# Optimization experiments

Hardware: AMD Instinct MI355X
Metric: run time of the kernel (lower is better)

## Reference

```python
import jax, jax.numpy as jnp
import numpy as np
from jax import lax

B, L, D, H = 32, 32, 512, 512
NEG = jnp.float32(-1e9)


def setup_inputs() -> dict:
    key = jax.random.key(0)
    k1, k2, k3, k4, k5 = jax.random.split(key, 5)
    return {
        "inp": jax.random.normal(k1, (B, L, D), jnp.float32),
        "length": jax.random.randint(k2, (B,), 2, L + 1),
        "W_word": jax.random.normal(k3, (D, 2 * H), jnp.float32) * np.float32(np.sqrt(2.0 / D)),
        "b_word": jnp.zeros((2 * H,), jnp.float32),
        "W_comp": jax.random.normal(k4, (2 * H, 5 * H), jnp.float32) * np.float32(np.sqrt(2.0 / (2 * H))),
        "b_comp": jnp.zeros((5 * H,), jnp.float32),
        "comp_query": jax.random.normal(k5, (H,), jnp.float32) * np.float32(0.01),
    }


def _forward(inp, length, W_word, b_word, W_comp, b_comp, comp_query):
    # length_mask[b, t] = 1 if t < length[b]
    length_mask = (jnp.arange(L)[None, :] < length[:, None]).astype(jnp.float32)  # (B, L)
    # leaf states from word_linear: (B, L, 2H) -> h, c
    hc = inp @ W_word + b_word
    h0, c0 = jnp.split(hc, 2, axis=-1)  # each (B, L, H)

    def cell(hl, cl, hr, cr):
        # BinaryTreeLSTMLayer: cat -> 5H gates
        g = jnp.concatenate([hl, hr], axis=-1) @ W_comp + b_comp  # (B, L-1, 5H)
        ig, fl, fr, u, o = jnp.split(g, 5, axis=-1)
        c = cl * jax.nn.sigmoid(fl + 1.0) + cr * jax.nn.sigmoid(fr + 1.0) + jnp.tanh(u) * jax.nn.sigmoid(ig)
        h = jax.nn.sigmoid(o) * jnp.tanh(c)
        return h, c

    def step(carry, i):
        # Fixed-shape (B, L, H) carry; valid length shrinks by 1 each step,
        # tail is zero-padded garbage never selected thanks to masks.
        h, c = carry
        hl, hr = h[:, :-1, :], h[:, 1:, :]
        cl, cr = c[:, :-1, :], c[:, 1:, :]
        nh, nc = cell(hl, cl, hr, cr)  # (B, L-1, H) candidate parents
        # greedy (eval-mode) top-1 composition selection
        logits = jnp.einsum('blh,h->bl', nh, comp_query)
        cand = (jnp.arange(L - 1)[None, :] < (length[:, None] - 1 - i)).astype(jnp.float32)
        sel = jax.nn.one_hot(jnp.argmax(jnp.where(cand > 0, logits, NEG), axis=1), L - 1, dtype=jnp.float32)
        cum = jnp.cumsum(sel, axis=1)
        left = 1.0 - cum
        right = jnp.concatenate([jnp.zeros((B, 1), jnp.float32), cum[:, :-1]], axis=1)
        ch = sel[..., None] * nh + left[..., None] * hl + right[..., None] * hr
        cc = sel[..., None] * nc + left[..., None] * cl + right[..., None] * cr
        sel_h = jnp.sum(sel[..., None] * ch, axis=1)  # (B, H) selected composed node
        is_last = (i == L - 2)  # final merge skips selection (single candidate)
        uh = jnp.where(is_last, nh, ch)
        uc = jnp.where(is_last, nc, cc)
        done = length_mask[:, i + 1][:, None, None]  # 1 if this sample still merging
        nhst = done * uh + (1.0 - done) * h[:, :-1, :]
        ncst = done * uc + (1.0 - done) * c[:, :-1, :]
        pad = jnp.zeros((B, 1, H), jnp.float32)
        h2 = jnp.concatenate([nhst, pad], axis=1)
        c2 = jnp.concatenate([ncst, pad], axis=1)
        node = jnp.where(is_last, h2[:, 0, :], sel_h)
        return (h2, c2), node

    (hf, cf), nodes_rest = lax.scan(step, (h0, c0), jnp.arange(L - 1))
    nodes = jnp.concatenate([h0, jnp.swapaxes(nodes_rest, 0, 1)], axis=1)  # (B, 2L-1, H)
    return hf[:, 0, :], cf[:, 0, :], nodes


def reference(inp, length, W_word, b_word, W_comp, b_comp, comp_query):
    return _forward(inp, length, W_word, b_word, W_comp, b_comp, comp_query)
```

## Files before the change

### kernel.cpp

```cpp
#include <hip/hip_runtime.h>
#include <math.h>

constexpr int NB = 32, NL = 32, ND = 512, NHID = 512, NSTEPS = 31;
constexpr int NC5 = 2560;
constexpr int BH = NB * NHID;
constexpr int HSLOT_Z = 32;
constexpr int NBLK = 160;
constexpr int NGEMM = 80;

constexpr float INV2048 = 1.f / 2048.f;

typedef _Float16 half8  __attribute__((ext_vector_type(8)));
typedef _Float16 half4  __attribute__((ext_vector_type(4)));
typedef float    f32x16 __attribute__((ext_vector_type(16)));
typedef unsigned long long u64;

constexpr size_t OFF_GRAW = 0;
constexpr size_t OFF_PNH  = OFF_GRAW + (size_t)32 * 32 * 2560;
constexpr size_t OFF_PNC  = OFF_PNH + (size_t)31 * 32 * 512;
constexpr size_t OFF_CST  = OFF_PNC + (size_t)31 * 32 * 512;
constexpr size_t OFF_HHI  = OFF_CST + (size_t)33 * 32 * 512;
constexpr size_t OFF_HLO  = OFF_HHI + (size_t)64 * 32 * 512 / 2;
constexpr size_t OFF_WTH  = OFF_HLO + (size_t)64 * 32 * 512 / 2;
constexpr size_t OFF_WTL  = OFF_WTH + (size_t)NC5 * 1024 / 2;
constexpr size_t OFF_INT  = OFF_WTL + (size_t)NC5 * 1024 / 2;
constexpr size_t OFF_LIST = OFF_INT + 8192;

__device__ __forceinline__ float sigf(float x) { return 1.f / (1.f + expf(-x)); }

__device__ __forceinline__ int ld_sc(const int* p) {
    return __hip_atomic_load(p, __ATOMIC_RELAXED, __HIP_MEMORY_SCOPE_AGENT);
}
__device__ __forceinline__ u64 ld_sc64(const void* p) {
    return __hip_atomic_load((const u64*)p, __ATOMIC_RELAXED, __HIP_MEMORY_SCOPE_AGENT);
}
__device__ __forceinline__ void st_sc64(void* p, u64 v) {
    __hip_atomic_store((u64*)p, v, __ATOMIC_RELAXED, __HIP_MEMORY_SCOPE_AGENT);
}
__device__ __forceinline__ u64 packf2(float a, float b) {
    return (u64)__float_as_uint(a) | ((u64)__float_as_uint(b) << 32);
}
__device__ __forceinline__ float2 uf2(u64 v) {
    float2 r;
    r.x = __uint_as_float((unsigned)v);
    r.y = __uint_as_float((unsigned)(v >> 32));
    return r;
}

__device__ __forceinline__ unsigned pack_e(int b, int slot, int l, int r) {
    return (unsigned)b | ((unsigned)slot << 5) | ((unsigned)l << 10) | ((unsigned)r << 16);
}

__global__ __launch_bounds__(256) void init_kernel(
    int* __restrict__ ireg, u64* __restrict__ elist,
    _Float16* __restrict__ hHi, _Float16* __restrict__ hLo, float* __restrict__ cSt)
{
    const int blk = blockIdx.x, tid = threadIdx.x;
    if (blk < 32) {
        if (tid < 31) {
            unsigned e = (unsigned)blk | ((unsigned)tid << 5) |
                         ((unsigned)tid << 10) | ((unsigned)(tid + 1) << 16);
            elist[tid * 32 + blk] = (u64)e;
        }
    } else if (blk == 32) {
        const size_t zb = (size_t)HSLOT_Z * NB * NHID;
        for (int i = tid; i < NB * NHID; i += 256) {
            hHi[zb + i] = (_Float16)0.f;
            hLo[zb + i] = (_Float16)0.f;
            cSt[zb + i] = 0.f;
        }
    } else {
        for (int i = tid; i < 8192; i += 256) ireg[i] = 0;
    }
}

__global__ __launch_bounds__(256) void wsplit_kernel(
    const float* __restrict__ W, _Float16* __restrict__ Wth, _Float16* __restrict__ Wtl)
{
    __shared__ float t[32][33];
    const int n0 = blockIdx.x * 32, k0 = blockIdx.y * 32;
    const int tid = threadIdx.x;
    const int c = tid & 31, r8 = tid >> 5;
#pragma unroll
    for (int p = 0; p < 4; ++p) {
        int r = p * 8 + r8;
        t[r][c] = W[(size_t)(k0 + r) * NC5 + n0 + c];
    }
    __syncthreads();
    const int nl = tid >> 3, k4 = (tid & 7) * 4;
    half4 vh, vl;
#pragma unroll
    for (int i = 0; i < 4; ++i) {
        float v = t[k4 + i][nl];
        _Float16 hh = (_Float16)v;
        vh[i] = hh;
        vl[i] = (_Float16)((v - (float)hh) * 2048.f);
    }
    size_t o = (size_t)(n0 + nl) * 1024 + k0 + k4;
    *(half4*)&Wth[o] = vh;
    *(half4*)&Wtl[o] = vl;
}

__global__ __launch_bounds__(256) void word_gemm64(
    const float* __restrict__ A, const float* __restrict__ W,
    const float* __restrict__ bias,
    _Float16* __restrict__ hi0, _Float16* __restrict__ lo0,
    float* __restrict__ cst, float* __restrict__ out)
{
    const int m0 = blockIdx.x * 64;
    const int n0 = blockIdx.y * 64;
    const int tid = threadIdx.x;
    const int tx = tid & 15, ty = tid >> 4;
    __shared__ float As[16][64];
    __shared__ float Bs[16][64];
    float acc[4][4];
#pragma unroll
    for (int i = 0; i < 4; ++i)
#pragma unroll
        for (int j = 0; j < 4; ++j) acc[i][j] = 0.f;

    for (int kt = 0; kt < ND; kt += 16) {
        {
            int row = tid >> 2, kq = tid & 3;
            float4 v = *(const float4*)(A + (size_t)(m0 + row) * ND + kt + kq * 4);
            As[kq * 4 + 0][row] = v.x;
            As[kq * 4 + 1][row] = v.y;
            As[kq * 4 + 2][row] = v.z;
            As[kq * 4 + 3][row] = v.w;
            int kr = tid >> 4, nq = tid & 15;
            float4 vb = *(const float4*)(W + (size_t)(kt + kr) * 1024 + n0 + nq * 4);
            *(float4*)&Bs[kr][nq * 4] = vb;
        }
        __syncthreads();
#pragma unroll
        for (int kk = 0; kk < 16; ++kk) {
            float a0 = As[kk][ty * 4 + 0], a1 = As[kk][ty * 4 + 1];
            float a2 = As[kk][ty * 4 + 2], a3 = As[kk][ty * 4 + 3];
            float4 bv = *(float4*)&Bs[kk][tx * 4];
            acc[0][0] = fmaf(a0, bv.x, acc[0][0]); acc[0][1] = fmaf(a0, bv.y, acc[0][1]);
            acc[0][2] = fmaf(a0, bv.z, acc[0][2]); acc[0][3] = fmaf(a0, bv.w, acc[0][3]);
            acc[1][0] = fmaf(a1, bv.x, acc[1][0]); acc[1][1] = fmaf(a1, bv.y, acc[1][1]);
            acc[1][2] = fmaf(a1, bv.z, acc[1][2]); acc[1][3] = fmaf(a1, bv.w, acc[1][3]);
            acc[2][0] = fmaf(a2, bv.x, acc[2][0]); acc[2][1] = fmaf(a2, bv.y, acc[2][1]);
            acc[2][2] = fmaf(a2, bv.z, acc[2][2]); acc[2][3] = fmaf(a2, bv.w, acc[2][3]);
            acc[3][0] = fmaf(a3, bv.x, acc[3][0]); acc[3][1] = fmaf(a3, bv.y, acc[3][1]);
            acc[3][2] = fmaf(a3, bv.z, acc[3][2]); acc[3][3] = fmaf(a3, bv.w, acc[3][3]);
        }
        __syncthreads();
    }
    float* nodes = out + 2 * BH;
#pragma unroll
    for (int i = 0; i < 4; ++i) {
        int r = m0 + ty * 4 + i;
        int b = r >> 5, l = r & 31;
#pragma unroll
        for (int jn = 0; jn < 4; ++jn) {
            int n = n0 + tx * 4 + jn;
            float v = acc[i][jn] + bias[n];
            if (n < NHID) {
                size_t si = ((size_t)l * NB + b) * NHID + n;
                _Float16 hh = (_Float16)v;
                hi0[si] = hh;
                lo0[si] = (_Float16)((v - (float)hh) * 2048.f);
                nodes[((size_t)b * 63 + l) * NHID + n] = v;
            } else {
                cst[((size_t)l * NB + b) * NHID + (n - NHID)] = v;
            }
        }
    }
}

__global__ __launch_bounds__(256, 1) void tree_loop(
    _Float16* __restrict__ hHi, _Float16* __restrict__ hLo,
    const _Float16* __restrict__ Wth, const _Float16* __restrict__ Wtl,
    float* __restrict__ graw, const float* __restrict__ bias,
    const float* __restrict__ q, const int* __restrict__ len,
    float* __restrict__ pnh, float* __restrict__ pnc, float* __restrict__ cSt,
    u64* __restrict__ elist, int* __restrict__ ireg, float* __restrict__ out)
{
    const int nt = blockIdx.x;
    const int tid = threadIdx.x;
    const int col = nt % NGEMM;
    const int kw = tid >> 6;
    const int lane = tid & 63;
    const int l5 = lane >> 5, ln = lane & 31;

    int* gd = ireg;

    __shared__ float red[4][32][32];
    __shared__ unsigned s_entry[64];
    __shared__ int s_pidx[32], s_hidx[32], s_cidx[32];
    __shared__ float s_plog[32];
    __shared__ int s_k;
    __shared__ int s_prevk;

    const _Float16* bHiP = Wth + (size_t)(col * 32 + ln) * 1024 + (kw << 8) + l5 * 8;
    const _Float16* bLoP = Wtl + (size_t)(col * 32 + ln) * 1024 + (kw << 8) + l5 * 8;
    half8 Bh[16], Bl[16];
#pragma unroll
    for (int ks = 0; ks < 16; ++ks) {
        Bh[ks] = *(const half8*)(bHiP + ks * 16);
        Bl[ks] = *(const half8*)(bLoP + ks * 16);
    }

    auto gemm_tile = [&](const unsigned* se) {
        {
            const unsigned e = se[ln];
            const int db = e & 31;
            const int lsl = (e >> 10) & 63, rsl = (e >> 16) & 63;
            const int hs = (kw < 2) ? lsl : rsl;
            const int koff = ((kw & 1) << 8) + l5 * 8;
            const _Float16* aHiP = hHi + ((size_t)hs * NB + db) * NHID + koff;
            const _Float16* aLoP = hLo + ((size_t)hs * NB + db) * NHID + koff;
            f32x16 acc1 = (f32x16)0.f, acc2 = (f32x16)0.f;
#pragma unroll
            for (int ks = 0; ks < 16; ++ks) {
                half8 Ah = *(const half8*)(aHiP + ks * 16);
                half8 Al = *(const half8*)(aLoP + ks * 16);
                acc1 = __builtin_amdgcn_mfma_f32_32x32x16_f16(Ah, Bh[ks], acc1, 0, 0, 0);
                acc2 = __builtin_amdgcn_mfma_f32_32x32x16_f16(Ah, Bl[ks], acc2, 0, 0, 0);
                acc2 = __builtin_amdgcn_mfma_f32_32x32x16_f16(Al, Bh[ks], acc2, 0, 0, 0);
            }
#pragma unroll
            for (int a = 0; a < 16; ++a) {
                int row = (a & 3) + 8 * (a >> 2) + 4 * l5;
                red[kw][row][ln] = acc1[a] + acc2[a] * INV2048;
            }
        }
        __syncthreads();
        {
            const int row = tid >> 3, c0 = (tid & 7) * 4;
            const unsigned er = se[row];
            const int rb = er & 31, rslot = (er >> 5) & 31;
            float4 s;
            s.x = (red[0][row][c0+0] + red[1][row][c0+0]) + (red[2][row][c0+0] + red[3][row][c0+0]);
            s.y = (red[0][row][c0+1] + red[1][row][c0+1]) + (red[2][row][c0+1] + red[3][row][c0+1]);
            s.z = (red[0][row][c0+2] + red[1][row][c0+2]) + (red[2][row][c0+2] + red[3][row][c0+2]);
            s.w = (red[0][row][c0+3] + red[1][row][c0+3]) + (red[2][row][c0+3] + red[3][row][c0+3]);
            float* gp = &graw[((size_t)rslot * NB + rb) * NC5 + col * 32 + c0];
            st_sc64(gp,     packf2(s.x, s.y));
            st_sc64(gp + 2, packf2(s.z, s.w));
        }
        __syncthreads();
    };

    __syncthreads();
    {
        const int par = nt / NGEMM;
        for (int mt = par; mt < 31; mt += 2) {
            if (tid < 32) s_entry[tid] = (unsigned)ld_sc64(&elist[mt * 32 + tid]);
            __syncthreads();
            gemm_tile(s_entry);
        }
        if (tid == 0) {
            asm volatile("s_waitcnt vmcnt(0)" ::: "memory");
            __hip_atomic_fetch_add(&gd[(nt & 3) * 32], 1, __ATOMIC_RELAXED,
                                   __HIP_MEMORY_SCOPE_AGENT);
        }
    }
    if (nt >= 112) return;

    if (nt < NGEMM) {
        for (int step = 1; step < NSTEPS; ++step) {
            if (tid < 64) {
                u64 e;
                while ((int)((e = ld_sc64(&elist[tid])) >> 32) < step)
                    __builtin_amdgcn_s_sleep(1);
                s_entry[tid] = (unsigned)e;
            }
            __syncthreads();
            gemm_tile(s_entry);
            gemm_tile(s_entry + 32);
            if (tid == 0) {
                asm volatile("s_waitcnt vmcnt(0)" ::: "memory");
                __hip_atomic_fetch_add(&gd[(nt & 3) * 32], 1, __ATOMIC_RELAXED,
                                       __HIP_MEMORY_SCOPE_AGENT);
            }
        }
        return;
    }

    {
        const int b = nt - NGEMM;
        const int lenb = len[b];
        if (tid < 32) { s_pidx[tid] = min(tid, 30); s_hidx[tid] = tid; s_cidx[tid] = tid; }
        if (tid == 0) s_prevk = -1;
        __syncthreads();

        for (int step = 0; step < NSTEPS; ++step) {
            if (tid < 4) {
                const int tgt = 40 + 20 * step;
                while (ld_sc(&gd[tid * 32]) < tgt) __builtin_amdgcn_s_sleep(1);
            }
            __syncthreads();

            const int pk = s_prevk;
            int nf;
            if (step == 0) nf = 31; else if (pk < 0) nf = 0; else nf = (pk >= 1) ? 2 : 1;
            for (int f = kw; f < nf; f += 4) {
                const int j = (step == 0) ? f : (pk - (nf - 1) + f);
                const int slot = s_pidx[j];
                const int lc = s_cidx[j], rc2 = s_cidx[j + 1];
                const float* gr  = graw + ((size_t)slot * NB + b) * NC5;
                const float* clp = cSt + ((size_t)lc * NB + b) * NHID;
                const float* crp = cSt + ((size_t)rc2 * NB + b) * NHID;
                float lpart = 0.f;
#pragma unroll
                for (int i = 0; i < 4; ++i) {
                    const int h = 2 * lane + 128 * i;
                    float2 g0 = uf2(ld_sc64(gr + h));
                    float2 g1 = uf2(ld_sc64(gr + 512 + h));
                    float2 g2 = uf2(ld_sc64(gr + 1024 + h));
                    float2 g3 = uf2(ld_sc64(gr + 1536 + h));
                    float2 g4 = uf2(ld_sc64(gr + 2048 + h));
                    const float2 b0 = *(const float2*)(bias + h);
                    const float2 b1 = *(const float2*)(bias + 512 + h);
                    const float2 b2 = *(const float2*)(bias + 1024 + h);
                    const float2 b3 = *(const float2*)(bias + 1536 + h);
                    const float2 b4 = *(const float2*)(bias + 2048 + h);
                    const float2 cl2 = *(const float2*)(clp + h);
                    const float2 cr2 = *(const float2*)(crp + h);
                    const float2 q2  = *(const float2*)(q + h);
                    float2 hv, cv;
                    {
                        float c = cl2.x * sigf(g1.x + b1.x + 1.f) + cr2.x * sigf(g2.x + b2.x + 1.f)
                                + tanhf(g3.x + b3.x) * sigf(g0.x + b0.x);
                        float hh = sigf(g4.x + b4.x) * tanhf(c);
                        cv.x = c; hv.x = hh;
                    }
                    {
                        float c = cl2.y * sigf(g1.y + b1.y + 1.f) + cr2.y * sigf(g2.y + b2.y + 1.f)
                                + tanhf(g3.y + b3.y) * sigf(g0.y + b0.y);
                        float hh = sigf(g4.y + b4.y) * tanhf(c);
                        cv.y = c; hv.y = hh;
                    }
                    const size_t po = ((size_t)slot * NB + b) * NHID + h;
                    *(float2*)(pnh + po) = hv;
                    *(float2*)(pnc + po) = cv;
                    lpart = fmaf(hv.x, q2.x, lpart);
                    lpart = fmaf(hv.y, q2.y, lpart);
                }
#pragma unroll
                for (int off = 32; off > 0; off >>= 1) lpart += __shfl_down(lpart, off);
                if (lane == 0) s_plog[slot] = lpart;
            }
            __syncthreads();

            const int actb = lenb - 1 - step;
            const int merge = actb >= 1;
            if (tid < 64) {
                float v = -1e30f;
                int idx = tid;
                if (tid < actb && tid < 31) v = s_plog[s_pidx[tid]];
#pragma unroll
                for (int off = 32; off > 0; off >>= 1) {
                    float ov = __shfl_down(v, off);
                    int   oi = __shfl_down(idx, off);
                    if (ov > v || (ov == v && oi < idx)) { v = ov; idx = oi; }
                }
                if (tid == 0) s_k = idx;
            }
            __syncthreads();
            const int k = s_k;
            const int last = (step == NSTEPS - 1);
            const int NSLOT = 33 + step;

            float* noderow = out + 2 * BH + ((size_t)b * 63 + 32 + step) * NHID;
            if (merge) {
                const int kslot = s_pidx[k];
                const int csl = s_cidx[k];
                if (tid < 128) {
                    const int h0 = tid * 4;
                    const size_t pb = ((size_t)kslot * NB + b) * NHID + h0;
                    float4 x4 = *(const float4*)&pnh[pb];
                    float4 c4 = *(const float4*)&pnc[pb];
                    half4 hv, lv;
#pragma unroll
                    for (int i = 0; i < 4; ++i) {
                        float x = (&x4.x)[i];
                        _Float16 hh = (_Float16)x;
                        hv[i] = hh;
                        lv[i] = (_Float16)((x - (float)hh) * 2048.f);
                    }
                    const size_t so = ((size_t)NSLOT * NB + b) * NHID + h0;
                    st_sc64(&hHi[so], __builtin_bit_cast(u64, hv));
                    st_sc64(&hLo[so], __builtin_bit_cast(u64, lv));
                    *(float4*)&cSt[((size_t)csl * NB + b) * NHID + h0] = c4;
                    *(float4*)&noderow[h0] = x4;
                    if (last) {
                        *(float4*)&out[b * NHID + h0] = x4;
                        *(float4*)&out[BH + b * NHID + h0] = c4;
                    }
                }
            } else {
                const int s0p = s_pidx[0], s0h = s_hidx[0], s0c = s_cidx[0];
                if (tid < 128) {
                    const int h0 = tid * 4;
                    if (!last) {
                        *(float4*)&noderow[h0] =
                            *(const float4*)&pnh[((size_t)s0p * NB + b) * NHID + h0];
                    } else {
                        const size_t so = ((size_t)s0h * NB + b) * NHID + h0;
                        half4 hv = __builtin_bit_cast(half4, ld_sc64(&hHi[so]));
                        half4 lv = __builtin_bit_cast(half4, ld_sc64(&hLo[so]));
                        float4 x4;
#pragma unroll
                        for (int i = 0; i < 4; ++i)
                            (&x4.x)[i] = (float)hv[i] + (float)lv[i] * INV2048;
                        *(float4*)&noderow[h0] = x4;
                        *(float4*)&out[b * NHID + h0] = x4;
                        *(float4*)&out[BH + b * NHID + h0] =
                            *(const float4*)&cSt[((size_t)s0c * NB + b) * NHID + h0];
                    }
                }
            }
            __syncthreads();

            if (tid == 0) {
                const unsigned dummy = pack_e(b, 31, HSLOT_Z, HSLOT_Z);
                if (merge) {
                    unsigned e1 = pack_e(b, s_pidx[k], NSLOT,
                                         (k + 2 <= 31) ? s_hidx[k + 2] : HSLOT_Z);
                    unsigned e0 = (k >= 1)
                        ? pack_e(b, s_pidx[k - 1], s_hidx[k - 1], NSLOT) : dummy;
                    if (!last) {
                        const u64 st = (u64)(step + 1) << 32;
                        st_sc64(&elist[2 * b],     (u64)e0 | st);
                        st_sc64(&elist[2 * b + 1], (u64)e1 | st);
                    }
                    const int recycP = s_pidx[k + 1];
                    for (int j2 = k + 1; j2 <= 29; ++j2) s_pidx[j2] = s_pidx[j2 + 1];
                    if (k < 30) s_pidx[30] = recycP;
                    s_hidx[k] = NSLOT;
                    for (int pp = k + 1; pp <= 30; ++pp) s_hidx[pp] = s_hidx[pp + 1];
                    s_hidx[31] = HSLOT_Z;
                    for (int pp = k + 1; pp <= 30; ++pp) s_cidx[pp] = s_cidx[pp + 1];
                    s_cidx[31] = HSLOT_Z;
                    s_prevk = k;
                } else {
                    if (!last) {
                        const u64 st = (u64)(step + 1) << 32;
                        st_sc64(&elist[2 * b],     (u64)dummy | st);
                        st_sc64(&elist[2 * b + 1], (u64)dummy | st);
                    }
                    s_prevk = -1;
                }
            }
        }
    }
}

extern "C" void kernel_launch(void* const* d_in, const int* in_sizes, int n_in,
                              void* d_out, int out_size, void* d_ws, size_t ws_size,
                              hipStream_t stream) {
    const float* inp    = (const float*)d_in[0];
    const int*   length = (const int*)d_in[1];
    const float* W_word = (const float*)d_in[2];
    const float* b_word = (const float*)d_in[3];
    const float* W_comp = (const float*)d_in[4];
    const float* b_comp = (const float*)d_in[5];
    const float* q      = (const float*)d_in[6];
    float* out = (float*)d_out;
    float* ws  = (float*)d_ws;

    float*     graw = ws + OFF_GRAW;
    float*     pnh  = ws + OFF_PNH;
    float*     pnc  = ws + OFF_PNC;
    float*     cSt  = ws + OFF_CST;
    _Float16*  hHi  = (_Float16*)(ws + OFF_HHI);
    _Float16*  hLo  = (_Float16*)(ws + OFF_HLO);
    _Float16*  Wth  = (_Float16*)(ws + OFF_WTH);
    _Float16*  Wtl  = (_Float16*)(ws + OFF_WTL);
    int*       ireg = (int*)(ws + OFF_INT);
    u64*       elist = (u64*)(ws + OFF_LIST);

    init_kernel<<<34, 256, 0, stream>>>(ireg, elist, hHi, hLo, cSt);
    wsplit_kernel<<<dim3(NC5 / 32, 1024 / 32), 256, 0, stream>>>(W_comp, Wth, Wtl);
    word_gemm64<<<dim3(16, 16), 256, 0, stream>>>(inp, W_word, b_word,
                                                  hHi, hLo, cSt, out);
    tree_loop<<<NBLK, 256, 0, stream>>>(hHi, hLo, Wth, Wtl, graw, b_comp, q, length,
                                        pnh, pnc, cSt, elist, ireg, out);
}
```

Baseline: 766.0 us.

## Split persistent tree loop into per-step kernel launches with pair GEMM prologue

Replaces the single persistent tree_loop kernel, which synchronised through spin-waits on step-tagged edge lists, with a pair_gemm0 kernel followed by 31 step_kernel launches. Per-batch tree bookkeeping (pidx/hidx/cidx/prevk) now lives in global memory between launches, and plogits move to a global buffer. Inside each step the first 32 blocks do the cell update and selection, then all 80 blocks wait on a counter before running the two-row GEMM. Kernel boundaries provide the cross-step ordering, which lets plain vector loads and stores replace some atomic accesses. In exchange each step pays launch overhead, reloads the weight fragments into registers, and re-reads the state from global memory.

```diff
diff --git a/kernel.cpp b/kernel.cpp
--- a/kernel.cpp
+++ b/kernel.cpp
@@ -1,12 +1,10 @@
 #include <hip/hip_runtime.h>
 #include <math.h>
 
-constexpr int NB = 32, NL = 32, ND = 512, NHID = 512, NSTEPS = 31;
+constexpr int NB = 32, ND = 512, NHID = 512, NSTEPS = 31;
 constexpr int NC5 = 2560;
 constexpr int BH = NB * NHID;
 constexpr int HSLOT_Z = 32;
-constexpr int NBLK = 160;
-constexpr int NGEMM = 80;
 
 constexpr float INV2048 = 1.f / 2048.f;
 
@@ -18,7 +16,8 @@
 constexpr size_t OFF_GRAW = 0;
 constexpr size_t OFF_PNH  = OFF_GRAW + (size_t)32 * 32 * 2560;
 constexpr size_t OFF_PNC  = OFF_PNH + (size_t)31 * 32 * 512;
-constexpr size_t OFF_CST  = OFF_PNC + (size_t)31 * 32 * 512;
+constexpr size_t OFF_PLOG = OFF_PNC + (size_t)31 * 32 * 512;
+constexpr size_t OFF_CST  = OFF_PLOG + 1024;
 constexpr size_t OFF_HHI  = OFF_CST + (size_t)33 * 32 * 512;
 constexpr size_t OFF_HLO  = OFF_HHI + (size_t)64 * 32 * 512 / 2;
 constexpr size_t OFF_WTH  = OFF_HLO + (size_t)64 * 32 * 512 / 2;
@@ -26,6 +25,13 @@
 constexpr size_t OFF_INT  = OFF_WTL + (size_t)NC5 * 1024 / 2;
 constexpr size_t OFF_LIST = OFF_INT + 8192;
 
+constexpr int IR_GD    = 0;
+constexpr int IR_PIDX  = 1024;
+constexpr int IR_HIDX  = 2048;
+constexpr int IR_CIDX  = 3072;
+constexpr int IR_PREVK = 4096;
+constexpr int IR_E0    = 5120;
+
 __device__ __forceinline__ float sigf(float x) { return 1.f / (1.f + expf(-x)); }
 
 __device__ __forceinline__ int ld_sc(const int* p) {
@@ -37,31 +43,24 @@
 __device__ __forceinline__ void st_sc64(void* p, u64 v) {
     __hip_atomic_store((u64*)p, v, __ATOMIC_RELAXED, __HIP_MEMORY_SCOPE_AGENT);
 }
-__device__ __forceinline__ u64 packf2(float a, float b) {
-    return (u64)__float_as_uint(a) | ((u64)__float_as_uint(b) << 32);
-}
-__device__ __forceinline__ float2 uf2(u64 v) {
-    float2 r;
-    r.x = __uint_as_float((unsigned)v);
-    r.y = __uint_as_float((unsigned)(v >> 32));
-    return r;
-}
-
 __device__ __forceinline__ unsigned pack_e(int b, int slot, int l, int r) {
     return (unsigned)b | ((unsigned)slot << 5) | ((unsigned)l << 10) | ((unsigned)r << 16);
 }
 
 __global__ __launch_bounds__(256) void init_kernel(
-    int* __restrict__ ireg, u64* __restrict__ elist,
+    int* __restrict__ ireg,
     _Float16* __restrict__ hHi, _Float16* __restrict__ hLo, float* __restrict__ cSt)
 {
     const int blk = blockIdx.x, tid = threadIdx.x;
     if (blk < 32) {
-        if (tid < 31) {
-            unsigned e = (unsigned)blk | ((unsigned)tid << 5) |
-                         ((unsigned)tid << 10) | ((unsigned)(tid + 1) << 16);
-            elist[tid * 32 + blk] = (u64)e;
-        }
+        if (tid < 32) {
+            ireg[IR_PIDX + blk * 32 + tid] = min(tid, 30);
+            ireg[IR_HIDX + blk * 32 + tid] = tid;
+            ireg[IR_CIDX + blk * 32 + tid] = tid;
+        }
+        if (tid == 0) ireg[IR_PREVK + blk] = -1;
+        if (tid < 31)
+            ireg[IR_E0 + tid * 32 + blk] = (int)pack_e(blk, tid, tid, tid + 1);
     } else if (blk == 32) {
         const size_t zb = (size_t)HSLOT_Z * NB * NHID;
         for (int i = tid; i < NB * NHID; i += 256) {
@@ -70,7 +69,7 @@
             cSt[zb + i] = 0.f;
         }
     } else {
-        for (int i = tid; i < 8192; i += 256) ireg[i] = 0;
+        if (tid < 128) ireg[IR_GD + tid] = 0;
     }
 }
 
@@ -170,30 +169,265 @@
     }
 }
 
-__global__ __launch_bounds__(256, 1) void tree_loop(
+__global__ __launch_bounds__(256, 1) void pair_gemm0(
+    const _Float16* __restrict__ hHi, const _Float16* __restrict__ hLo,
+    const _Float16* __restrict__ Wth, const _Float16* __restrict__ Wtl,
+    const int* __restrict__ ireg, float* __restrict__ graw)
+{
+    const int col = blockIdx.x, g = blockIdx.y;
+    const int tid = threadIdx.x;
+    const int kw = tid >> 6, lane = tid & 63;
+    const int l5 = lane >> 5, ln = lane & 31;
+    __shared__ float red[4][32][32];
+    __shared__ unsigned s_entry[32];
+
+    const _Float16* bHiP = Wth + (size_t)(col * 32 + ln) * 1024 + (kw << 8) + l5 * 8;
+    const _Float16* bLoP = Wtl + (size_t)(col * 32 + ln) * 1024 + (kw << 8) + l5 * 8;
+    half8 Bh[16], Bl[16];
+#pragma unroll
+    for (int ks = 0; ks < 16; ++ks) {
+        Bh[ks] = *(const half8*)(bHiP + ks * 16);
+        Bl[ks] = *(const half8*)(bLoP + ks * 16);
+    }
+
+    const int mt0 = g * 8, mt1 = min(mt0 + 8, 31);
+    for (int mt = mt0; mt < mt1; ++mt) {
+        if (tid < 32) s_entry[tid] = (unsigned)ireg[IR_E0 + mt * 32 + tid];
+        __syncthreads();
+        {
+            const unsigned e = s_entry[ln];
+            const int db = e & 31;
+            const int lsl = (e >> 10) & 63, rsl = (e >> 16) & 63;
+            const int hs = (kw < 2) ? lsl : rsl;
+            const int koff = ((kw & 1) << 8) + l5 * 8;
+            const _Float16* aHiP = hHi + ((size_t)hs * NB + db) * NHID + koff;
+            const _Float16* aLoP = hLo + ((size_t)hs * NB + db) * NHID + koff;
+            f32x16 acc1 = (f32x16)0.f, acc2 = (f32x16)0.f;
+#pragma unroll
+            for (int ks = 0; ks < 16; ++ks) {
+                half8 Ah = *(const half8*)(aHiP + ks * 16);
+                half8 Al = *(const half8*)(aLoP + ks * 16);
+                acc1 = __builtin_amdgcn_mfma_f32_32x32x16_f16(Ah, Bh[ks], acc1, 0, 0, 0);
+                acc2 = __builtin_amdgcn_mfma_f32_32x32x16_f16(Ah, Bl[ks], acc2, 0, 0, 0);
+                acc2 = __builtin_amdgcn_mfma_f32_32x32x16_f16(Al, Bh[ks], acc2, 0, 0, 0);
+            }
+#pragma unroll
+            for (int a = 0; a < 16; ++a) {
+                int row = (a & 3) + 8 * (a >> 2) + 4 * l5;
+                red[kw][row][ln] = acc1[a] + acc2[a] * INV2048;
+            }
+        }
+        __syncthreads();
+        {
+            const int row = tid >> 3, c0 = (tid & 7) * 4;
+            const unsigned er = s_entry[row];
+            const int rb = er & 31, rslot = (er >> 5) & 31;
+            float4 s;
+            s.x = (red[0][row][c0+0] + red[1][row][c0+0]) + (red[2][row][c0+0] + red[3][row][c0+0]);
+            s.y = (red[0][row][c0+1] + red[1][row][c0+1]) + (red[2][row][c0+1] + red[3][row][c0+1]);
+            s.z = (red[0][row][c0+2] + red[1][row][c0+2]) + (red[2][row][c0+2] + red[3][row][c0+2]);
+            s.w = (red[0][row][c0+3] + red[1][row][c0+3]) + (red[2][row][c0+3] + red[3][row][c0+3]);
+            *(float4*)&graw[((size_t)rslot * NB + rb) * NC5 + col * 32 + c0] = s;
+        }
+        __syncthreads();
+    }
+}
+
+__global__ __launch_bounds__(256, 1) void step_kernel(
     _Float16* __restrict__ hHi, _Float16* __restrict__ hLo,
     const _Float16* __restrict__ Wth, const _Float16* __restrict__ Wtl,
     float* __restrict__ graw, const float* __restrict__ bias,
     const float* __restrict__ q, const int* __restrict__ len,
-    float* __restrict__ pnh, float* __restrict__ pnc, float* __restrict__ cSt,
-    u64* __restrict__ elist, int* __restrict__ ireg, float* __restrict__ out)
+    float* __restrict__ pnh, float* __restrict__ pnc, float* __restrict__ plogG,
+    float* __restrict__ cSt, u64* __restrict__ elist64,
+    int* __restrict__ ireg, float* __restrict__ out, int step)
 {
     const int nt = blockIdx.x;
     const int tid = threadIdx.x;
-    const int col = nt % NGEMM;
-    const int kw = tid >> 6;
-    const int lane = tid & 63;
+    const int kw = tid >> 6, lane = tid & 63;
     const int l5 = lane >> 5, ln = lane & 31;
-
-    int* gd = ireg;
+    const int last = (step == NSTEPS - 1);
+
+    int* gd = ireg + IR_GD;
 
     __shared__ float red[4][32][32];
     __shared__ unsigned s_entry[64];
     __shared__ int s_pidx[32], s_hidx[32], s_cidx[32];
-    __shared__ float s_plog[32];
-    __shared__ int s_k;
-    __shared__ int s_prevk;
-
+    __shared__ int s_k, s_prevk;
+
+    if (nt < NB) {
+        const int b = nt;
+        if (tid < 32) {
+            s_pidx[tid] = ireg[IR_PIDX + b * 32 + tid];
+            s_hidx[tid] = ireg[IR_HIDX + b * 32 + tid];
+            s_cidx[tid] = ireg[IR_CIDX + b * 32 + tid];
+        }
+        if (tid == 0) s_prevk = ireg[IR_PREVK + b];
+        const int lenb = len[b];
+        __syncthreads();
+
+        const int pk = s_prevk;
+        int nf;
+        if (step == 0) nf = 31; else if (pk < 0) nf = 0; else nf = (pk >= 1) ? 2 : 1;
+
+        for (int f = kw; f < nf; f += 4) {
+            const int j = (step == 0) ? f : (pk - (nf - 1) + f);
+            const int slot = s_pidx[j];
+            const int lc = s_cidx[j], rc2 = s_cidx[j + 1];
+            const float* gr  = graw + ((size_t)slot * NB + b) * NC5;
+            const float* clp = cSt + ((size_t)lc * NB + b) * NHID;
+            const float* crp = cSt + ((size_t)rc2 * NB + b) * NHID;
+            float lpart = 0.f;
+#pragma unroll
+            for (int i = 0; i < 2; ++i) {
+                const int h = 4 * lane + 256 * i;
+                float4 g0 = *(const float4*)(gr + h);
+                float4 g1 = *(const float4*)(gr + 512 + h);
+                float4 g2 = *(const float4*)(gr + 1024 + h);
+                float4 g3 = *(const float4*)(gr + 1536 + h);
+                float4 g4 = *(const float4*)(gr + 2048 + h);
+                const float4 b0 = *(const float4*)(bias + h);
+                const float4 b1 = *(const float4*)(bias + 512 + h);
+                const float4 b2 = *(const float4*)(bias + 1024 + h);
+                const float4 b3 = *(const float4*)(bias + 1536 + h);
+                const float4 b4 = *(const float4*)(bias + 2048 + h);
+                const float4 cl4 = *(const float4*)(clp + h);
+                const float4 cr4 = *(const float4*)(crp + h);
+                const float4 q4  = *(const float4*)(q + h);
+                float4 hv, cv;
+#define CELL(e) { \
+                float c = cl4.e * sigf(g1.e + b1.e + 1.f) + cr4.e * sigf(g2.e + b2.e + 1.f) \
+                        + tanhf(g3.e + b3.e) * sigf(g0.e + b0.e); \
+                float hh = sigf(g4.e + b4.e) * tanhf(c); \
+                cv.e = c; hv.e = hh; lpart = fmaf(hh, q4.e, lpart); }
+                CELL(x) CELL(y) CELL(z) CELL(w)
+#undef CELL
+                const size_t po = ((size_t)slot * NB + b) * NHID + h;
+                *(float4*)(pnh + po) = hv;
+                *(float4*)(pnc + po) = cv;
+            }
+#pragma unroll
+            for (int off = 32; off > 0; off >>= 1) lpart += __shfl_down(lpart, off);
+            if (lane == 0) plogG[b * 32 + slot] = lpart;
+        }
+        __syncthreads();
+
+        const int actb = lenb - 1 - step;
+        const int merge = actb >= 1;
+        if (tid < 64) {
+            float v = -1e30f;
+            int idx = tid;
+            if (tid < actb && tid < 31) v = plogG[b * 32 + s_pidx[tid]];
+#pragma unroll
+            for (int off = 32; off > 0; off >>= 1) {
+                float ov = __shfl_down(v, off);
+                int   oi = __shfl_down(idx, off);
+                if (ov > v || (ov == v && oi < idx)) { v = ov; idx = oi; }
+            }
+            if (tid == 0) s_k = idx;
+        }
+        __syncthreads();
+        const int k = s_k;
+        const int NSLOT = 33 + step;
+
+        float* noderow = out + 2 * BH + ((size_t)b * 63 + 32 + step) * NHID;
+        if (merge) {
+            const int kslot = s_pidx[k];
+            const int csl = s_cidx[k];
+            if (tid < 128) {
+                const int h0 = tid * 4;
+                const size_t pb = ((size_t)kslot * NB + b) * NHID + h0;
+                float4 x4 = *(const float4*)&pnh[pb];
+                float4 c4 = *(const float4*)&pnc[pb];
+                half4 hv, lv;
+#pragma unroll
+                for (int i = 0; i < 4; ++i) {
+                    float x = (&x4.x)[i];
+                    _Float16 hh = (_Float16)x;
+                    hv[i] = hh;
+                    lv[i] = (_Float16)((x - (float)hh) * 2048.f);
+                }
+                const size_t so = ((size_t)NSLOT * NB + b) * NHID + h0;
+                st_sc64(&hHi[so], __builtin_bit_cast(u64, hv));
+                st_sc64(&hLo[so], __builtin_bit_cast(u64, lv));
+                *(float4*)&cSt[((size_t)csl * NB + b) * NHID + h0] = c4;
+                *(float4*)&noderow[h0] = x4;
+                if (last) {
+                    *(float4*)&out[b * NHID + h0] = x4;
+                    *(float4*)&out[BH + b * NHID + h0] = c4;
+                }
+            }
+        } else {
+            const int s0p = s_pidx[0], s0h = s_hidx[0], s0c = s_cidx[0];
+            if (tid < 128) {
+                const int h0 = tid * 4;
+                if (!last) {
+                    *(float4*)&noderow[h0] =
+                        *(const float4*)&pnh[((size_t)s0p * NB + b) * NHID + h0];
+                } else {
+                    const size_t so = ((size_t)s0h * NB + b) * NHID + h0;
+                    half4 hv = *(const half4*)&hHi[so];
+                    half4 lv = *(const half4*)&hLo[so];
+                    float4 x4;
+#pragma unroll
+                    for (int i = 0; i < 4; ++i)
+                        (&x4.x)[i] = (float)hv[i] + (float)lv[i] * INV2048;
+                    *(float4*)&noderow[h0] = x4;
+                    *(float4*)&out[b * NHID + h0] = x4;
+                    *(float4*)&out[BH + b * NHID + h0] =
+                        *(const float4*)&cSt[((size_t)s0c * NB + b) * NHID + h0];
+                }
+            }
+        }
+        __syncthreads();
+
+        if (tid == 0) {
+            const unsigned dummy = pack_e(b, 31, HSLOT_Z, HSLOT_Z);
+            if (merge) {
+                unsigned e1 = pack_e(b, s_pidx[k], NSLOT,
+                                     (k + 2 <= 31) ? s_hidx[k + 2] : HSLOT_Z);
+                unsigned e0 = (k >= 1)
+                    ? pack_e(b, s_pidx[k - 1], s_hidx[k - 1], NSLOT) : dummy;
+                if (!last) {
+                    st_sc64(&elist64[2 * b],     (u64)e0);
+                    st_sc64(&elist64[2 * b + 1], (u64)e1);
+                }
+                const int recycP = s_pidx[k + 1];
+                for (int j2 = k + 1; j2 <= 29; ++j2) s_pidx[j2] = s_pidx[j2 + 1];
+                if (k < 30) s_pidx[30] = recycP;
+                s_hidx[k] = NSLOT;
+                for (int pp = k + 1; pp <= 30; ++pp) s_hidx[pp] = s_hidx[pp + 1];
+                s_hidx[31] = HSLOT_Z;
+                for (int pp = k + 1; pp <= 30; ++pp) s_cidx[pp] = s_cidx[pp + 1];
+                s_cidx[31] = HSLOT_Z;
+                s_prevk = k;
+            } else {
+                if (!last) {
+                    st_sc64(&elist64[2 * b],     (u64)dummy);
+                    st_sc64(&elist64[2 * b + 1], (u64)dummy);
+                }
+                s_prevk = -1;
+            }
+        }
+        __syncthreads();
+        if (tid < 32) {
+            ireg[IR_PIDX + b * 32 + tid] = s_pidx[tid];
+            ireg[IR_HIDX + b * 32 + tid] = s_hidx[tid];
+            ireg[IR_CIDX + b * 32 + tid] = s_cidx[tid];
+        }
+        if (tid == 0) {
+            ireg[IR_PREVK + b] = s_prevk;
+            if (!last) {
+                asm volatile("s_waitcnt vmcnt(0)" ::: "memory");
+                __hip_atomic_fetch_add(&gd[(b & 3) * 32], 1, __ATOMIC_RELAXED,
+                                       __HIP_MEMORY_SCOPE_AGENT);
+            }
+        }
+    }
+
+    if (last) return;
+
+    const int col = nt;
     const _Float16* bHiP = Wth + (size_t)(col * 32 + ln) * 1024 + (kw << 8) + l5 * 8;
     const _Float16* bLoP = Wtl + (size_t)(col * 32 + ln) * 1024 + (kw << 8) + l5 * 8;
     half8 Bh[16], Bl[16];
@@ -203,7 +437,17 @@
         Bl[ks] = *(const half8*)(bLoP + ks * 16);
     }
 
-    auto gemm_tile = [&](const unsigned* se) {
+    if (tid < 4) {
+        const int tgt = 8 * (step + 1);
+        while (ld_sc(&gd[tid * 32]) < tgt) __builtin_amdgcn_s_sleep(1);
+    }
+    __syncthreads();
+    if (tid < 64) s_entry[tid] = (unsigned)ld_sc64(&elist64[tid]);
+    __syncthreads();
+
+#pragma unroll
+    for (int half = 0; half < 2; ++half) {
+        const unsigned* se = s_entry + half * 32;
         {
             const unsigned e = se[ln];
             const int db = e & 31;
@@ -237,216 +481,9 @@
             s.y = (red[0][row][c0+1] + red[1][row][c0+1]) + (red[2][row][c0+1] + red[3][row][c0+1]);
             s.z = (red[0][row][c0+2] + red[1][row][c0+2]) + (red[2][row][c0+2] + red[3][row][c0+2]);
             s.w = (red[0][row][c0+3] + red[1][row][c0+3]) + (red[2][row][c0+3] + red[3][row][c0+3]);
-            float* gp = &graw[((size_t)rslot * NB + rb) * NC5 + col * 32 + c0];
-            st_sc64(gp,     packf2(s.x, s.y));
-            st_sc64(gp + 2, packf2(s.z, s.w));
-        }
-        __syncthreads();
-    };
-
-    __syncthreads();
-    {
-        const int par = nt / NGEMM;
-        for (int mt = par; mt < 31; mt += 2) {
-            if (tid < 32) s_entry[tid] = (unsigned)ld_sc64(&elist[mt * 32 + tid]);
-            __syncthreads();
-            gemm_tile(s_entry);
-        }
-        if (tid == 0) {
-            asm volatile("s_waitcnt vmcnt(0)" ::: "memory");
-            __hip_atomic_fetch_add(&gd[(nt & 3) * 32], 1, __ATOMIC_RELAXED,
-                                   __HIP_MEMORY_SCOPE_AGENT);
-        }
-    }
-    if (nt >= 112) return;
-
-    if (nt < NGEMM) {
-        for (int step = 1; step < NSTEPS; ++step) {
-            if (tid < 64) {
-                u64 e;
-                while ((int)((e = ld_sc64(&elist[tid])) >> 32) < step)
-                    __builtin_amdgcn_s_sleep(1);
-                s_entry[tid] = (unsigned)e;
-            }
-            __syncthreads();
-            gemm_tile(s_entry);
-            gemm_tile(s_entry + 32);
-            if (tid == 0) {
-                asm volatile("s_waitcnt vmcnt(0)" ::: "memory");
-                __hip_atomic_fetch_add(&gd[(nt & 3) * 32], 1, __ATOMIC_RELAXED,
-                                       __HIP_MEMORY_SCOPE_AGENT);
-            }
-        }
-        return;
-    }
-
-    {
-        const int b = nt - NGEMM;
-        const int lenb = len[b];
-        if (tid < 32) { s_pidx[tid] = min(tid, 30); s_hidx[tid] = tid; s_cidx[tid] = tid; }
-        if (tid == 0) s_prevk = -1;
-        __syncthreads();
-
-        for (int step = 0; step < NSTEPS; ++step) {
-            if (tid < 4) {
-                const int tgt = 40 + 20 * step;
-                while (ld_sc(&gd[tid * 32]) < tgt) __builtin_amdgcn_s_sleep(1);
-            }
-            __syncthreads();
-
-            const int pk = s_prevk;
-            int nf;
-            if (step == 0) nf = 31; else if (pk < 0) nf = 0; else nf = (pk >= 1) ? 2 : 1;
-            for (int f = kw; f < nf; f += 4) {
-                const int j = (step == 0) ? f : (pk - (nf - 1) + f);
-                const int slot = s_pidx[j];
-                const int lc = s_cidx[j], rc2 = s_cidx[j + 1];
-                const float* gr  = graw + ((size_t)slot * NB + b) * NC5;
-                const float* clp = cSt + ((size_t)lc * NB + b) * NHID;
-                const float* crp = cSt + ((size_t)rc2 * NB + b) * NHID;
-                float lpart = 0.f;
-#pragma unroll
-                for (int i = 0; i < 4; ++i) {
-                    const int h = 2 * lane + 128 * i;
-                    float2 g0 = uf2(ld_sc64(gr + h));
-                    float2 g1 = uf2(ld_sc64(gr + 512 + h));
-                    float2 g2 = uf2(ld_sc64(gr + 1024 + h));
-                    float2 g3 = uf2(ld_sc64(gr + 1536 + h));
-                    float2 g4 = uf2(ld_sc64(gr + 2048 + h));
-                    const float2 b0 = *(const float2*)(bias + h);
-                    const float2 b1 = *(const float2*)(bias + 512 + h);
-                    const float2 b2 = *(const float2*)(bias + 1024 + h);
-                    const float2 b3 = *(const float2*)(bias + 1536 + h);
-                    const float2 b4 = *(const float2*)(bias + 2048 + h);
-                    const float2 cl2 = *(const float2*)(clp + h);
-                    const float2 cr2 = *(const float2*)(crp + h);
-                    const float2 q2  = *(const float2*)(q + h);
-                    float2 hv, cv;
-                    {
-                        float c = cl2.x * sigf(g1.x + b1.x + 1.f) + cr2.x * sigf(g2.x + b2.x + 1.f)
-                                + tanhf(g3.x + b3.x) * sigf(g0.x + b0.x);
-                        float hh = sigf(g4.x + b4.x) * tanhf(c);
-                        cv.x = c; hv.x = hh;
-                    }
-                    {
-                        float c = cl2.y * sigf(g1.y + b1.y + 1.f) + cr2.y * sigf(g2.y + b2.y + 1.f)
-                                + tanhf(g3.y + b3.y) * sigf(g0.y + b0.y);
-                        float hh = sigf(g4.y + b4.y) * tanhf(c);
-                        cv.y = c; hv.y = hh;
-                    }
-                    const size_t po = ((size_t)slot * NB + b) * NHID + h;
-                    *(float2*)(pnh + po) = hv;
-                    *(float2*)(pnc + po) = cv;
-                    lpart = fmaf(hv.x, q2.x, lpart);
-                    lpart = fmaf(hv.y, q2.y, lpart);
-                }
-#pragma unroll
-                for (int off = 32; off > 0; off >>= 1) lpart += __shfl_down(lpart, off);
-                if (lane == 0) s_plog[slot] = lpart;
-            }
-            __syncthreads();
-
-            const int actb = lenb - 1 - step;
-            const int merge = actb >= 1;
-            if (tid < 64) {
-                float v = -1e30f;
-                int idx = tid;
-                if (tid < actb && tid < 31) v = s_plog[s_pidx[tid]];
-#pragma unroll
-                for (int off = 32; off > 0; off >>= 1) {
-                    float ov = __shfl_down(v, off);
-                    int   oi = __shfl_down(idx, off);
-                    if (ov > v || (ov == v && oi < idx)) { v = ov; idx = oi; }
-                }
-                if (tid == 0) s_k = idx;
-            }
-            __syncthreads();
-            const int k = s_k;
-            const int last = (step == NSTEPS - 1);
-            const int NSLOT = 33 + step;
-
-            float* noderow = out + 2 * BH + ((size_t)b * 63 + 32 + step) * NHID;
-            if (merge) {
-                const int kslot = s_pidx[k];
-                const int csl = s_cidx[k];
-                if (tid < 128) {
-                    const int h0 = tid * 4;
-                    const size_t pb = ((size_t)kslot * NB + b) * NHID + h0;
-                    float4 x4 = *(const float4*)&pnh[pb];
-                    float4 c4 = *(const float4*)&pnc[pb];
-                    half4 hv, lv;
-#pragma unroll
-                    for (int i = 0; i < 4; ++i) {
-                        float x = (&x4.x)[i];
-                        _Float16 hh = (_Float16)x;
-                        hv[i] = hh;
-                        lv[i] = (_Float16)((x - (float)hh) * 2048.f);
-                    }
-                    const size_t so = ((size_t)NSLOT * NB + b) * NHID + h0;
-                    st_sc64(&hHi[so], __builtin_bit_cast(u64, hv));
-                    st_sc64(&hLo[so], __builtin_bit_cast(u64, lv));
-                    *(float4*)&cSt[((size_t)csl * NB + b) * NHID + h0] = c4;
-                    *(float4*)&noderow[h0] = x4;
-                    if (last) {
-                        *(float4*)&out[b * NHID + h0] = x4;
-                        *(float4*)&out[BH + b * NHID + h0] = c4;
-                    }
-                }
-            } else {
-                const int s0p = s_pidx[0], s0h = s_hidx[0], s0c = s_cidx[0];
-                if (tid < 128) {
-                    const int h0 = tid * 4;
-                    if (!last) {
-                        *(float4*)&noderow[h0] =
-                            *(const float4*)&pnh[((size_t)s0p * NB + b) * NHID + h0];
-                    } else {
-                        const size_t so = ((size_t)s0h * NB + b) * NHID + h0;
-                        half4 hv = __builtin_bit_cast(half4, ld_sc64(&hHi[so]));
-                        half4 lv = __builtin_bit_cast(half4, ld_sc64(&hLo[so]));
-                        float4 x4;
-#pragma unroll
-                        for (int i = 0; i < 4; ++i)
-                            (&x4.x)[i] = (float)hv[i] + (float)lv[i] * INV2048;
-                        *(float4*)&noderow[h0] = x4;
-                        *(float4*)&out[b * NHID + h0] = x4;
-                        *(float4*)&out[BH + b * NHID + h0] =
-                            *(const float4*)&cSt[((size_t)s0c * NB + b) * NHID + h0];
-                    }
-                }
-            }
-            __syncthreads();
-
-            if (tid == 0) {
-                const unsigned dummy = pack_e(b, 31, HSLOT_Z, HSLOT_Z);
-                if (merge) {
-                    unsigned e1 = pack_e(b, s_pidx[k], NSLOT,
-                                         (k + 2 <= 31) ? s_hidx[k + 2] : HSLOT_Z);
-                    unsigned e0 = (k >= 1)
-                        ? pack_e(b, s_pidx[k - 1], s_hidx[k - 1], NSLOT) : dummy;
-                    if (!last) {
-                        const u64 st = (u64)(step + 1) << 32;
-                        st_sc64(&elist[2 * b],     (u64)e0 | st);
-                        st_sc64(&elist[2 * b + 1], (u64)e1 | st);
-                    }
-                    const int recycP = s_pidx[k + 1];
-                    for (int j2 = k + 1; j2 <= 29; ++j2) s_pidx[j2] = s_pidx[j2 + 1];
-                    if (k < 30) s_pidx[30] = recycP;
-                    s_hidx[k] = NSLOT;
-                    for (int pp = k + 1; pp <= 30; ++pp) s_hidx[pp] = s_hidx[pp + 1];
-                    s_hidx[31] = HSLOT_Z;
-                    for (int pp = k + 1; pp <= 30; ++pp) s_cidx[pp] = s_cidx[pp + 1];
-                    s_cidx[31] = HSLOT_Z;
-                    s_prevk = k;
-                } else {
-                    if (!last) {
-                        const u64 st = (u64)(step + 1) << 32;
-                        st_sc64(&elist[2 * b],     (u64)dummy | st);
-                        st_sc64(&elist[2 * b + 1], (u64)dummy | st);
-                    }
-                    s_prevk = -1;
-                }
-            }
-        }
+            *(float4*)&graw[((size_t)rslot * NB + rb) * NC5 + col * 32 + c0] = s;
+        }
+        __syncthreads();
     }
 }
 
@@ -466,18 +503,24 @@
     float*     graw = ws + OFF_GRAW;
     float*     pnh  = ws + OFF_PNH;
     float*     pnc  = ws + OFF_PNC;
+    float*     plog = ws + OFF_PLOG;
     float*     cSt  = ws + OFF_CST;
     _Float16*  hHi  = (_Float16*)(ws + OFF_HHI);
     _Float16*  hLo  = (_Float16*)(ws + OFF_HLO);
     _Float16*  Wth  = (_Float16*)(ws + OFF_WTH);
     _Float16*  Wtl  = (_Float16*)(ws + OFF_WTL);
     int*       ireg = (int*)(ws + OFF_INT);
-    u64*       elist = (u64*)(ws + OFF_LIST);
-
-    init_kernel<<<34, 256, 0, stream>>>(ireg, elist, hHi, hLo, cSt);
+    u64*       elist64 = (u64*)(ws + OFF_LIST);
+
+    init_kernel<<<34, 256, 0, stream>>>(ireg, hHi, hLo, cSt);
     wsplit_kernel<<<dim3(NC5 / 32, 1024 / 32), 256, 0, stream>>>(W_comp, Wth, Wtl);
     word_gemm64<<<dim3(16, 16), 256, 0, stream>>>(inp, W_word, b_word,
                                                   hHi, hLo, cSt, out);
-    tree_loop<<<NBLK, 256, 0, stream>>>(hHi, hLo, Wth, Wtl, graw, b_comp, q, length,
-                                        pnh, pnc, cSt, elist, ireg, out);
-}
+    pair_gemm0<<<dim3(80, 4), 256, 0, stream>>>(hHi, hLo, Wth, Wtl, ireg, graw);
+    for (int i = 0; i < NSTEPS; ++i) {
+        const int grid = (i == NSTEPS - 1) ? 32 : 80;
+        step_kernel<<<grid, 256, 0, stream>>>(
+            hHi, hLo, Wth, Wtl, graw, b_comp, q, length,
+            pnh, pnc, plog, cSt, elist64, ireg, out, i);
+    }
+}
```

Measured after the change: 819.1 us. 1.07x slower.
